# Kernel tuning notes

Measured on AMD Instinct MI355X. Metric: run time of the kernel, lower is better.

The kernel has to match this reference:

```python
import jax, jax.numpy as jnp
import numpy as np

N_NODES = 10000
N_EDGES = 640000
HIDDEN = 128
N_LAYERS = 3
DECAY_RATE = 1.0


def setup_inputs() -> dict:
    key = jax.random.key(0)
    ks = jax.random.split(key, 16)
    D, L = HIDDEN, N_LAYERS
    s = 1.0 / np.sqrt(D)
    inp = {
        "x": jax.random.normal(ks[0], (N_NODES, D), dtype=jnp.float32),
        "edge_index": jax.random.randint(ks[1], (2, N_EDGES), 0, N_NODES, dtype=jnp.int32),
        "confidences": jax.random.uniform(ks[2], (N_NODES,), dtype=jnp.float32),
        # per-layer message MLP params, stacked over layers: [L, D, D] / [L, D]
        "msg_W1": jax.random.normal(ks[3], (L, D, D), dtype=jnp.float32) * s,
        "msg_b1": jnp.zeros((L, D), dtype=jnp.float32),
        "msg_W2": jax.random.normal(ks[4], (L, D, D), dtype=jnp.float32) * s,
        "msg_b2": jnp.zeros((L, D), dtype=jnp.float32),
        # per-layer self MLP params
        "self_W1": jax.random.normal(ks[5], (L, D, D), dtype=jnp.float32) * s,
        "self_b1": jnp.zeros((L, D), dtype=jnp.float32),
        "self_W2": jax.random.normal(ks[6], (L, D, D), dtype=jnp.float32) * s,
        "self_b2": jnp.zeros((L, D), dtype=jnp.float32),
        # layer-importance score net: Linear(D,D) -> ReLU -> Linear(D,1)
        "score_W1": jax.random.normal(ks[7], (D, D), dtype=jnp.float32) * s,
        "score_b1": jnp.zeros((D,), dtype=jnp.float32),
        "score_W2": jax.random.normal(ks[8], (D, 1), dtype=jnp.float32) * s,
        "score_b2": jnp.zeros((1,), dtype=jnp.float32),
    }
    return inp


def _mlp2(h, W1, b1, W2, b2):
    return jax.nn.relu(h @ W1 + b1) @ W2 + b2


def reference(x, edge_index, confidences,
              msg_W1, msg_b1, msg_W2, msg_b2,
              self_W1, self_b1, self_W2, self_b2,
              score_W1, score_b1, score_W2, score_b2):
    src, dst = edge_index[0], edge_index[1]
    # confidence-weighted edge weights: exp(-decay * |c_src - c_dst|)
    edge_weights = jnp.exp(-DECAY_RATE * jnp.abs(confidences[src] - confidences[dst]))  # [E]

    h = x
    layer_outputs = []
    for i in range(N_LAYERS):
        messages = _mlp2(h[src], msg_W1[i], msg_b1[i], msg_W2[i], msg_b2[i])  # [E, D]
        messages = messages * edge_weights[:, None]
        aggr = jax.ops.segment_sum(messages, dst, num_segments=N_NODES)  # [N, D]
        self_loop = _mlp2(h, self_W1[i], self_b1[i], self_W2[i], self_b2[i])
        h = jax.nn.relu(aggr + self_loop)  # dropout is identity in eval mode
        layer_outputs.append(h)

    stacked = jnp.stack(layer_outputs, axis=0)  # [L, N, D]
    scores = _mlp2(stacked, score_W1, score_b1, score_W2, score_b2)[..., 0]  # [L, N]
    layer_weights = jax.nn.softmax(scores, axis=0)  # softmax over layers
    output = jnp.sum(layer_weights[:, :, None] * stacked, axis=0)  # [N, D]
    return output, stacked, layer_weights
```

## Files before the change

kernel.cpp:

```cpp
#include <hip/hip_runtime.h>
#include <hip/hip_fp16.h>

#define NN 10000
#define NE 640000
#define D 128
#define NF (NN * D)
#define WS 136
#define CAP 128
#define GMB 157
#define GE ((NE + 255) / 256)
#define NAGG (NN / 4)
#define NDZ ((NN + 255) / 256)

typedef __bf16 bf16x8 __attribute__((ext_vector_type(8)));
typedef float f32x4 __attribute__((ext_vector_type(4)));


__global__ __launch_bounds__(256) void prep_kernel(
    const float* __restrict__ mW1, const float* __restrict__ mW2,
    const float* __restrict__ sW1, const float* __restrict__ sW2,
    const float* __restrict__ scW1, __bf16* __restrict__ wt, int* __restrict__ deg) {
    int b = blockIdx.x, t = threadIdx.x;
    if (b < 13) {
        int m = b;
        const float* W = (m < 3)   ? mW1 + (size_t)m * D * D
                       : (m < 6)   ? mW2 + (size_t)(m - 3) * D * D
                       : (m < 9)   ? sW1 + (size_t)(m - 6) * D * D
                       : (m < 12)  ? sW2 + (size_t)(m - 9) * D * D
                                   : scW1;
        __bf16* o = wt + (size_t)m * D * WS;
        for (int i = t; i < D * D; i += 256) {
            int k = i >> 7, n = i & 127;
            o[n * WS + k] = (__bf16)W[i];
        }
    } else {
        int i = (b - 13) * 256 + t;
        if (i < NN) deg[i] = 0;
    }
}


__device__ __forceinline__ void mlp_nostage_body(
    const __bf16* __restrict__ Abf, const float* __restrict__ Af32,
    const __bf16* __restrict__ Wt1, const float* __restrict__ b1,
    const __bf16* __restrict__ Wt2, const float* __restrict__ b2,
    __bf16* __restrict__ Mbf, float* __restrict__ Cself, int write_bf,
    __bf16 (*Tl)[16 * WS], int bx, int t) {
    int wid = t >> 6, lane = t & 63;
    int m16 = lane & 15, q = lane >> 4;
    int row0 = bx * 64 + wid * 16;
    int arow = min(row0 + m16, NN - 1);

    bf16x8 af[4];
    if (Af32) {
#pragma unroll
        for (int kk = 0; kk < 4; kk++) {
            const float4* pa = (const float4*)&Af32[(size_t)arow * D + kk * 32 + q * 8];
            float4 v0 = pa[0], v1 = pa[1];
            bf16x8 f;
            f[0] = (__bf16)v0.x; f[1] = (__bf16)v0.y; f[2] = (__bf16)v0.z; f[3] = (__bf16)v0.w;
            f[4] = (__bf16)v1.x; f[5] = (__bf16)v1.y; f[6] = (__bf16)v1.z; f[7] = (__bf16)v1.w;
            af[kk] = f;
        }
    } else {
#pragma unroll
        for (int kk = 0; kk < 4; kk++)
            af[kk] = *(const bf16x8*)&Abf[(size_t)arow * D + kk * 32 + q * 8];
    }
    float b1v[8], b2v[8];
#pragma unroll
    for (int ct = 0; ct < 8; ct++) { b1v[ct] = b1[ct * 16 + m16]; b2v[ct] = b2[ct * 16 + m16]; }

    f32x4 acc[8];
#pragma unroll
    for (int ct = 0; ct < 8; ct++) acc[ct] = (f32x4){0.f, 0.f, 0.f, 0.f};
#pragma unroll
    for (int kk = 0; kk < 4; kk++) {
#pragma unroll
        for (int ct = 0; ct < 8; ct++) {
            bf16x8 bb = *(const bf16x8*)&Wt1[(ct * 16 + m16) * WS + kk * 32 + q * 8];
            acc[ct] = __builtin_amdgcn_mfma_f32_16x16x32_bf16(af[kk], bb, acc[ct], 0, 0, 0);
        }
    }
#pragma unroll
    for (int ct = 0; ct < 8; ct++) {
#pragma unroll
        for (int r = 0; r < 4; r++) {
            float v = fmaxf(acc[ct][r] + b1v[ct], 0.f);
            Tl[wid][(q * 4 + r) * WS + ct * 16 + m16] = (__bf16)v;
        }
    }
#pragma unroll
    for (int ct = 0; ct < 8; ct++) acc[ct] = (f32x4){0.f, 0.f, 0.f, 0.f};
#pragma unroll
    for (int kk = 0; kk < 4; kk++) {
        bf16x8 a = *(const bf16x8*)&Tl[wid][m16 * WS + kk * 32 + q * 8];
#pragma unroll
        for (int ct = 0; ct < 8; ct++) {
            bf16x8 bb = *(const bf16x8*)&Wt2[(ct * 16 + m16) * WS + kk * 32 + q * 8];
            acc[ct] = __builtin_amdgcn_mfma_f32_16x16x32_bf16(a, bb, acc[ct], 0, 0, 0);
        }
    }
    if (write_bf) {
#pragma unroll
        for (int ct = 0; ct < 8; ct++) {
#pragma unroll
            for (int r = 0; r < 4; r++) {
                int row = row0 + q * 4 + r;
                if (row < NN) Mbf[(size_t)row * D + ct * 16 + m16] = (__bf16)(acc[ct][r] + b2v[ct]);
            }
        }
    } else {
#pragma unroll
        for (int ct = 0; ct < 8; ct++) {
#pragma unroll
            for (int r = 0; r < 4; r++) {
                int row = row0 + q * 4 + r;
                if (row < NN) Cself[(size_t)row * D + ct * 16 + m16] = acc[ct][r] + b2v[ct];
            }
        }
    }
}


__global__ __launch_bounds__(256) void scatter_mlp0_kernel(
    const int* __restrict__ ei, const float* __restrict__ conf,
    int* __restrict__ deg, unsigned* __restrict__ meta,
    const float* __restrict__ x,
    const __bf16* __restrict__ wt, const float* __restrict__ b1m, const float* __restrict__ b2m,
    const float* __restrict__ b1s, const float* __restrict__ b2s,
    __bf16* __restrict__ Mbf, float* __restrict__ Cself) {
    __shared__ __align__(16) __bf16 Tl[4][16 * WS];
    const size_t MAT = (size_t)D * WS;
    int b = blockIdx.x, t = threadIdx.x;
    if (b < GE) {
        int e = b * 256 + t;
        if (e < NE) {
            int s = ei[e];
            int d = ei[NE + e];
            float w = expf(-fabsf(conf[s] - conf[d]));
            __half h = __float2half(w);
            unsigned short us = *reinterpret_cast<unsigned short*>(&h);
            unsigned v = ((unsigned)s << 16) | us;
            int r = atomicAdd(&deg[d], 1);
            if (r < CAP) meta[(size_t)d * CAP + r] = v;
        }
        return;
    }
    int mb = b - GE;
    if (mb < GMB)
        mlp_nostage_body(nullptr, x, wt + 0 * MAT, b1m, wt + 3 * MAT, b2m,
                         Mbf, nullptr, 1, Tl, mb, t);
    else
        mlp_nostage_body(nullptr, x, wt + 6 * MAT, b1s, wt + 9 * MAT, b2s,
                         nullptr, Cself, 0, Tl, mb - GMB, t);
}


__device__ __forceinline__ void agg_gather(
    const uint4* __restrict__ Mbf4, const int* __restrict__ deg,
    const unsigned* __restrict__ meta, int wid, int lane, float a[8]) {
    int q = lane >> 4, l4 = lane & 15, l5 = lane & 31;
    int dg = min(deg[wid], CAP);
    size_t beg = (size_t)wid * CAP;
#pragma unroll
    for (int i = 0; i < 8; i++) a[i] = 0.f;
    unsigned mcur = meta[beg + l5];
    for (int rel = 0; rel < dg; rel += 32) {
        unsigned mnext = meta[beg + rel + 32 + l5];
        int srcid[8];
        float wgt[8];
#pragma unroll
        for (int u = 0; u < 8; u++) {
            int sl = 4 * u + q;
            unsigned v = __shfl((int)mcur, sl);
            bool valid = (rel + sl) < dg;
            srcid[u] = valid ? (int)(v >> 16) : 0;
            unsigned short us = (unsigned short)(v & 0xFFFFu);
            __half h = *reinterpret_cast<__half*>(&us);
            wgt[u] = valid ? __half2float(h) : 0.f;
        }
        uint4 g[8];
#pragma unroll
        for (int u = 0; u < 8; u++) g[u] = Mbf4[(size_t)srcid[u] * 16 + l4];
#pragma unroll
        for (int u = 0; u < 8; u++) {
            float w = wgt[u];
            a[0] = fmaf(w, __uint_as_float(g[u].x << 16), a[0]);
            a[1] = fmaf(w, __uint_as_float(g[u].x & 0xFFFF0000u), a[1]);
            a[2] = fmaf(w, __uint_as_float(g[u].y << 16), a[2]);
            a[3] = fmaf(w, __uint_as_float(g[u].y & 0xFFFF0000u), a[3]);
            a[4] = fmaf(w, __uint_as_float(g[u].z << 16), a[4]);
            a[5] = fmaf(w, __uint_as_float(g[u].z & 0xFFFF0000u), a[5]);
            a[6] = fmaf(w, __uint_as_float(g[u].w << 16), a[6]);
            a[7] = fmaf(w, __uint_as_float(g[u].w & 0xFFFF0000u), a[7]);
        }
        mcur = mnext;
    }
#pragma unroll
    for (int i = 0; i < 8; i++) {
        a[i] += __shfl_xor(a[i], 16);
        a[i] += __shfl_xor(a[i], 32);
    }
}


__global__ __launch_bounds__(256) void aggregate_kernel(
    const uint4* __restrict__ Mbf4, const float4* __restrict__ Mself4,
    const int* __restrict__ deg, const unsigned* __restrict__ meta,
    float4* __restrict__ out4, bf16x8* __restrict__ stbf8) {
    int wid = (blockIdx.x * 256 + threadIdx.x) >> 6;
    int lane = threadIdx.x & 63;
    int q = lane >> 4, l4 = lane & 15;
    float a[8];
    agg_gather(Mbf4, deg, meta, wid, lane, a);
    if (q == 0) {
        float4 sv0 = Mself4[(size_t)wid * 32 + 2 * l4];
        float4 sv1 = Mself4[(size_t)wid * 32 + 2 * l4 + 1];
        float4 r0, r1;
        r0.x = fmaxf(a[0] + sv0.x, 0.f);
        r0.y = fmaxf(a[1] + sv0.y, 0.f);
        r0.z = fmaxf(a[2] + sv0.z, 0.f);
        r0.w = fmaxf(a[3] + sv0.w, 0.f);
        r1.x = fmaxf(a[4] + sv1.x, 0.f);
        r1.y = fmaxf(a[5] + sv1.y, 0.f);
        r1.z = fmaxf(a[6] + sv1.z, 0.f);
        r1.w = fmaxf(a[7] + sv1.w, 0.f);
        out4[(size_t)wid * 32 + 2 * l4] = r0;
        out4[(size_t)wid * 32 + 2 * l4 + 1] = r1;
        bf16x8 hb;
        hb[0] = (__bf16)r0.x; hb[1] = (__bf16)r0.y;
        hb[2] = (__bf16)r0.z; hb[3] = (__bf16)r0.w;
        hb[4] = (__bf16)r1.x; hb[5] = (__bf16)r1.y;
        hb[6] = (__bf16)r1.z; hb[7] = (__bf16)r1.w;
        stbf8[(size_t)wid * 16 + l4] = hb;
    }
}


__global__ __launch_bounds__(256) void mlp_pair_mfma(
    const __bf16* __restrict__ Abf,
    const __bf16* __restrict__ Wt1a, const float* __restrict__ b1a,
    const __bf16* __restrict__ Wt2a, const float* __restrict__ b2a, __bf16* __restrict__ Mbf,
    const __bf16* __restrict__ Wt1b, const float* __restrict__ b1b,
    const __bf16* __restrict__ Wt2b, const float* __restrict__ b2b, float* __restrict__ Cself) {
    __shared__ __align__(16) __bf16 Tl[4][16 * WS];
    int pb = blockIdx.y;
    mlp_nostage_body(Abf, nullptr,
                     pb ? Wt1b : Wt1a, pb ? b1b : b1a,
                     pb ? Wt2b : Wt2a, pb ? b2b : b2a,
                     Mbf, Cself, pb == 0, Tl, blockIdx.x, threadIdx.x);
}


__global__ __launch_bounds__(256) void score_finalize_mfma(
    const __bf16* __restrict__ stbf, const float* __restrict__ st,
    const __bf16* __restrict__ Wt1, const float* __restrict__ b1,
    const float* __restrict__ w2, const float* __restrict__ b2,
    float* __restrict__ out, float* __restrict__ lw_out) {
    __shared__ float sc_l[3][64];
    __shared__ float lw_l[3][64];
    int t = threadIdx.x;
    int wid = t >> 6, lane = t & 63;
    int m16 = lane & 15, q = lane >> 4;
    int row0 = blockIdx.x * 64;

    int arow = min(row0 + wid * 16 + m16, NN - 1);
    float bb = b2[0];

    for (int l = 0; l < 3; l++) {
        const __bf16* A = stbf + (size_t)l * NF;
        f32x4 acc[8];
#pragma unroll
        for (int ct = 0; ct < 8; ct++) acc[ct] = (f32x4){0.f, 0.f, 0.f, 0.f};
#pragma unroll
        for (int kk = 0; kk < 4; kk++) {
            bf16x8 a = *(const bf16x8*)&A[(size_t)arow * D + kk * 32 + q * 8];
#pragma unroll
            for (int ct = 0; ct < 8; ct++) {
                bf16x8 b = *(const bf16x8*)&Wt1[(ct * 16 + m16) * WS + kk * 32 + q * 8];
                acc[ct] = __builtin_amdgcn_mfma_f32_16x16x32_bf16(a, b, acc[ct], 0, 0, 0);
            }
        }
        float p[4] = {0.f, 0.f, 0.f, 0.f};
#pragma unroll
        for (int ct = 0; ct < 8; ct++) {
            float bv = b1[ct * 16 + m16];
            float wv = w2[ct * 16 + m16];
#pragma unroll
            for (int r = 0; r < 4; r++) p[r] += fmaxf(acc[ct][r] + bv, 0.f) * wv;
        }
#pragma unroll
        for (int r = 0; r < 4; r++) {
#pragma unroll
            for (int off = 1; off < 16; off <<= 1) p[r] += __shfl_xor(p[r], off);
            if (m16 == 0) sc_l[l][wid * 16 + q * 4 + r] = p[r] + bb;
        }
    }
    __syncthreads();

    if (t < 64) {
        int row = row0 + t;
        float s0 = sc_l[0][t], s1 = sc_l[1][t], s2 = sc_l[2][t];
        float m = fmaxf(s0, fmaxf(s1, s2));
        float e0 = expf(s0 - m), e1 = expf(s1 - m), e2 = expf(s2 - m);
        float inv = 1.f / (e0 + e1 + e2);
        lw_l[0][t] = e0 * inv;
        lw_l[1][t] = e1 * inv;
        lw_l[2][t] = e2 * inv;
        if (row < NN) {
            lw_out[row] = e0 * inv;
            lw_out[NN + row] = e1 * inv;
            lw_out[2 * NN + row] = e2 * inv;
        }
    }
    __syncthreads();

    for (int i = t; i < 64 * 32; i += 256) {
        int r = i >> 5, c4 = i & 31;
        int row = row0 + r;
        if (row >= NN) break;
        float4 v0 = ((const float4*)(st + (size_t)row * D))[c4];
        float4 v1 = ((const float4*)(st + (size_t)NF + (size_t)row * D))[c4];
        float4 v2 = ((const float4*)(st + 2 * (size_t)NF + (size_t)row * D))[c4];
        float w0 = lw_l[0][r], w1 = lw_l[1][r], w2v = lw_l[2][r];
        float4 o;
        o.x = w0 * v0.x + w1 * v1.x + w2v * v2.x;
        o.y = w0 * v0.y + w1 * v1.y + w2v * v2.y;
        o.z = w0 * v0.z + w1 * v1.z + w2v * v2.z;
        o.w = w0 * v0.w + w1 * v1.w + w2v * v2.w;
        ((float4*)(out + (size_t)row * D))[c4] = o;
    }
}

extern "C" void kernel_launch(void* const* d_in, const int* in_sizes, int n_in,
                              void* d_out, int out_size, void* d_ws, size_t ws_size,
                              hipStream_t stream) {
    const float* x = (const float*)d_in[0];
    const int* ei = (const int*)d_in[1];
    const float* conf = (const float*)d_in[2];
    const float* msg_W1 = (const float*)d_in[3];
    const float* msg_b1 = (const float*)d_in[4];
    const float* msg_W2 = (const float*)d_in[5];
    const float* msg_b2 = (const float*)d_in[6];
    const float* self_W1 = (const float*)d_in[7];
    const float* self_b1 = (const float*)d_in[8];
    const float* self_W2 = (const float*)d_in[9];
    const float* self_b2 = (const float*)d_in[10];
    const float* score_W1 = (const float*)d_in[11];
    const float* score_b1 = (const float*)d_in[12];
    const float* score_W2 = (const float*)d_in[13];
    const float* score_b2 = (const float*)d_in[14];

    float* out = (float*)d_out;
    float* out_stacked = out + NF;
    float* out_lw = out + 4 * (size_t)NF;

    float* w = (float*)d_ws;
    float* Mself = w;
    unsigned* meta = (unsigned*)(Mself + (size_t)NF);
    __bf16* stbf = (__bf16*)(meta + (size_t)NN * CAP + 64);
    __bf16* Mbf = stbf + 3 * (size_t)NF;
    __bf16* wt = Mbf + (size_t)NF;
    int* deg = (int*)(wt + 13 * (size_t)D * WS);

    const size_t MAT = (size_t)D * WS;

    prep_kernel<<<13 + NDZ, 256, 0, stream>>>(
        msg_W1, msg_W2, self_W1, self_W2, score_W1, wt, deg);
    scatter_mlp0_kernel<<<GE + 2 * GMB, 256, 0, stream>>>(
        ei, conf, deg, meta, x, wt, msg_b1, msg_b2, self_b1, self_b2, Mbf, Mself);
    aggregate_kernel<<<NAGG, 256, 0, stream>>>(
        (const uint4*)Mbf, (const float4*)Mself, deg, meta,
        (float4*)(out_stacked + 0 * (size_t)NF), (bf16x8*)(stbf + 0 * (size_t)NF));
    mlp_pair_mfma<<<dim3(GMB, 2), 256, 0, stream>>>(
        stbf + 0 * (size_t)NF,
        wt + 1 * MAT, msg_b1 + D, wt + 4 * MAT, msg_b2 + D, Mbf,
        wt + 7 * MAT, self_b1 + D, wt + 10 * MAT, self_b2 + D, Mself);
    aggregate_kernel<<<NAGG, 256, 0, stream>>>(
        (const uint4*)Mbf, (const float4*)Mself, deg, meta,
        (float4*)(out_stacked + 1 * (size_t)NF), (bf16x8*)(stbf + 1 * (size_t)NF));
    mlp_pair_mfma<<<dim3(GMB, 2), 256, 0, stream>>>(
        stbf + 1 * (size_t)NF,
        wt + 2 * MAT, msg_b1 + 2 * D, wt + 5 * MAT, msg_b2 + 2 * D, Mbf,
        wt + 8 * MAT, self_b1 + 2 * D, wt + 11 * MAT, self_b2 + 2 * D, Mself);
    aggregate_kernel<<<NAGG, 256, 0, stream>>>(
        (const uint4*)Mbf, (const float4*)Mself, deg, meta,
        (float4*)(out_stacked + 2 * (size_t)NF), (bf16x8*)(stbf + 2 * (size_t)NF));
    score_finalize_mfma<<<GMB, 256, 0, stream>>>(
        stbf, out_stacked, wt + 12 * MAT, score_b1, score_W2, score_b2, out, out_lw);
}
```

Measured before the change: 271.2 us.

## Fuse message and self MLPs per block and store full-precision edge metadata

Each block now runs both the message MLP and the self MLP on the same input rows, so the A fragment is loaded and converted once instead of twice, and the launch grid is halved. In the first kernel the MLP blocks now come before the edge-scatter blocks. The edge metadata changes from a packed 16-bit source plus fp16 weight to a float2 holding the source id and an fp32 weight. This removes the half-precision conversion but doubles the metadata footprint read during every aggregation.

```diff
diff --git a/kernel.cpp b/kernel.cpp
--- a/kernel.cpp
+++ b/kernel.cpp
@@ -1,5 +1,4 @@
 #include <hip/hip_runtime.h>
-#include <hip/hip_fp16.h>
 
 #define NN 10000
 #define NE 640000
@@ -40,11 +39,74 @@
 }
 
 
-__device__ __forceinline__ void mlp_nostage_body(
-    const __bf16* __restrict__ Abf, const float* __restrict__ Af32,
+__device__ __forceinline__ void mlp_half(
+    const bf16x8 af[4],
     const __bf16* __restrict__ Wt1, const float* __restrict__ b1,
     const __bf16* __restrict__ Wt2, const float* __restrict__ b2,
     __bf16* __restrict__ Mbf, float* __restrict__ Cself, int write_bf,
+    __bf16* Tlw, int row0, int m16, int q) {
+    float b1v[8], b2v[8];
+#pragma unroll
+    for (int ct = 0; ct < 8; ct++) { b1v[ct] = b1[ct * 16 + m16]; b2v[ct] = b2[ct * 16 + m16]; }
+
+    f32x4 acc[8];
+#pragma unroll
+    for (int ct = 0; ct < 8; ct++) acc[ct] = (f32x4){0.f, 0.f, 0.f, 0.f};
+#pragma unroll
+    for (int kk = 0; kk < 4; kk++) {
+#pragma unroll
+        for (int ct = 0; ct < 8; ct++) {
+            bf16x8 bb = *(const bf16x8*)&Wt1[(ct * 16 + m16) * WS + kk * 32 + q * 8];
+            acc[ct] = __builtin_amdgcn_mfma_f32_16x16x32_bf16(af[kk], bb, acc[ct], 0, 0, 0);
+        }
+    }
+#pragma unroll
+    for (int ct = 0; ct < 8; ct++) {
+#pragma unroll
+        for (int r = 0; r < 4; r++) {
+            float v = fmaxf(acc[ct][r] + b1v[ct], 0.f);
+            Tlw[(q * 4 + r) * WS + ct * 16 + m16] = (__bf16)v;
+        }
+    }
+#pragma unroll
+    for (int ct = 0; ct < 8; ct++) acc[ct] = (f32x4){0.f, 0.f, 0.f, 0.f};
+#pragma unroll
+    for (int kk = 0; kk < 4; kk++) {
+        bf16x8 a = *(const bf16x8*)&Tlw[m16 * WS + kk * 32 + q * 8];
+#pragma unroll
+        for (int ct = 0; ct < 8; ct++) {
+            bf16x8 bb = *(const bf16x8*)&Wt2[(ct * 16 + m16) * WS + kk * 32 + q * 8];
+            acc[ct] = __builtin_amdgcn_mfma_f32_16x16x32_bf16(a, bb, acc[ct], 0, 0, 0);
+        }
+    }
+    if (write_bf) {
+#pragma unroll
+        for (int ct = 0; ct < 8; ct++) {
+#pragma unroll
+            for (int r = 0; r < 4; r++) {
+                int row = row0 + q * 4 + r;
+                if (row < NN) Mbf[(size_t)row * D + ct * 16 + m16] = (__bf16)(acc[ct][r] + b2v[ct]);
+            }
+        }
+    } else {
+#pragma unroll
+        for (int ct = 0; ct < 8; ct++) {
+#pragma unroll
+            for (int r = 0; r < 4; r++) {
+                int row = row0 + q * 4 + r;
+                if (row < NN) Cself[(size_t)row * D + ct * 16 + m16] = acc[ct][r] + b2v[ct];
+            }
+        }
+    }
+}
+
+
+__device__ __forceinline__ void mlp_dual_body(
+    const __bf16* __restrict__ Abf, const float* __restrict__ Af32,
+    const __bf16* __restrict__ Wt1m, const float* __restrict__ b1m,
+    const __bf16* __restrict__ Wt2m, const float* __restrict__ b2m, __bf16* __restrict__ Mbf,
+    const __bf16* __restrict__ Wt1s, const float* __restrict__ b1s,
+    const __bf16* __restrict__ Wt2s, const float* __restrict__ b2s, float* __restrict__ Cself,
     __bf16 (*Tl)[16 * WS], int bx, int t) {
     int wid = t >> 6, lane = t & 63;
     int m16 = lane & 15, q = lane >> 4;
@@ -67,65 +129,14 @@
         for (int kk = 0; kk < 4; kk++)
             af[kk] = *(const bf16x8*)&Abf[(size_t)arow * D + kk * 32 + q * 8];
     }
-    float b1v[8], b2v[8];
-#pragma unroll
-    for (int ct = 0; ct < 8; ct++) { b1v[ct] = b1[ct * 16 + m16]; b2v[ct] = b2[ct * 16 + m16]; }
-
-    f32x4 acc[8];
-#pragma unroll
-    for (int ct = 0; ct < 8; ct++) acc[ct] = (f32x4){0.f, 0.f, 0.f, 0.f};
-#pragma unroll
-    for (int kk = 0; kk < 4; kk++) {
-#pragma unroll
-        for (int ct = 0; ct < 8; ct++) {
-            bf16x8 bb = *(const bf16x8*)&Wt1[(ct * 16 + m16) * WS + kk * 32 + q * 8];
-            acc[ct] = __builtin_amdgcn_mfma_f32_16x16x32_bf16(af[kk], bb, acc[ct], 0, 0, 0);
-        }
-    }
-#pragma unroll
-    for (int ct = 0; ct < 8; ct++) {
-#pragma unroll
-        for (int r = 0; r < 4; r++) {
-            float v = fmaxf(acc[ct][r] + b1v[ct], 0.f);
-            Tl[wid][(q * 4 + r) * WS + ct * 16 + m16] = (__bf16)v;
-        }
-    }
-#pragma unroll
-    for (int ct = 0; ct < 8; ct++) acc[ct] = (f32x4){0.f, 0.f, 0.f, 0.f};
-#pragma unroll
-    for (int kk = 0; kk < 4; kk++) {
-        bf16x8 a = *(const bf16x8*)&Tl[wid][m16 * WS + kk * 32 + q * 8];
-#pragma unroll
-        for (int ct = 0; ct < 8; ct++) {
-            bf16x8 bb = *(const bf16x8*)&Wt2[(ct * 16 + m16) * WS + kk * 32 + q * 8];
-            acc[ct] = __builtin_amdgcn_mfma_f32_16x16x32_bf16(a, bb, acc[ct], 0, 0, 0);
-        }
-    }
-    if (write_bf) {
-#pragma unroll
-        for (int ct = 0; ct < 8; ct++) {
-#pragma unroll
-            for (int r = 0; r < 4; r++) {
-                int row = row0 + q * 4 + r;
-                if (row < NN) Mbf[(size_t)row * D + ct * 16 + m16] = (__bf16)(acc[ct][r] + b2v[ct]);
-            }
-        }
-    } else {
-#pragma unroll
-        for (int ct = 0; ct < 8; ct++) {
-#pragma unroll
-            for (int r = 0; r < 4; r++) {
-                int row = row0 + q * 4 + r;
-                if (row < NN) Cself[(size_t)row * D + ct * 16 + m16] = acc[ct][r] + b2v[ct];
-            }
-        }
-    }
+    mlp_half(af, Wt1m, b1m, Wt2m, b2m, Mbf, nullptr, 1, Tl[wid], row0, m16, q);
+    mlp_half(af, Wt1s, b1s, Wt2s, b2s, nullptr, Cself, 0, Tl[wid], row0, m16, q);
 }
 
 
 __global__ __launch_bounds__(256) void scatter_mlp0_kernel(
     const int* __restrict__ ei, const float* __restrict__ conf,
-    int* __restrict__ deg, unsigned* __restrict__ meta,
+    int* __restrict__ deg, float2* __restrict__ meta,
     const float* __restrict__ x,
     const __bf16* __restrict__ wt, const float* __restrict__ b1m, const float* __restrict__ b2m,
     const float* __restrict__ b1s, const float* __restrict__ b2s,
@@ -133,52 +144,44 @@
     __shared__ __align__(16) __bf16 Tl[4][16 * WS];
     const size_t MAT = (size_t)D * WS;
     int b = blockIdx.x, t = threadIdx.x;
-    if (b < GE) {
-        int e = b * 256 + t;
-        if (e < NE) {
-            int s = ei[e];
-            int d = ei[NE + e];
-            float w = expf(-fabsf(conf[s] - conf[d]));
-            __half h = __float2half(w);
-            unsigned short us = *reinterpret_cast<unsigned short*>(&h);
-            unsigned v = ((unsigned)s << 16) | us;
-            int r = atomicAdd(&deg[d], 1);
-            if (r < CAP) meta[(size_t)d * CAP + r] = v;
-        }
+    if (b < GMB) {
+        mlp_dual_body(nullptr, x,
+                      wt + 0 * MAT, b1m, wt + 3 * MAT, b2m, Mbf,
+                      wt + 6 * MAT, b1s, wt + 9 * MAT, b2s, Cself, Tl, b, t);
         return;
     }
-    int mb = b - GE;
-    if (mb < GMB)
-        mlp_nostage_body(nullptr, x, wt + 0 * MAT, b1m, wt + 3 * MAT, b2m,
-                         Mbf, nullptr, 1, Tl, mb, t);
-    else
-        mlp_nostage_body(nullptr, x, wt + 6 * MAT, b1s, wt + 9 * MAT, b2s,
-                         nullptr, Cself, 0, Tl, mb - GMB, t);
+    int e = (b - GMB) * 256 + t;
+    if (e < NE) {
+        int s = ei[e];
+        int d = ei[NE + e];
+        float w = expf(-fabsf(conf[s] - conf[d]));
+        int r = atomicAdd(&deg[d], 1);
+        if (r < CAP) meta[(size_t)d * CAP + r] = make_float2(__int_as_float(s), w);
+    }
 }
 
 
 __device__ __forceinline__ void agg_gather(
     const uint4* __restrict__ Mbf4, const int* __restrict__ deg,
-    const unsigned* __restrict__ meta, int wid, int lane, float a[8]) {
+    const float2* __restrict__ meta, int wid, int lane, float a[8]) {
     int q = lane >> 4, l4 = lane & 15, l5 = lane & 31;
     int dg = min(deg[wid], CAP);
     size_t beg = (size_t)wid * CAP;
 #pragma unroll
     for (int i = 0; i < 8; i++) a[i] = 0.f;
-    unsigned mcur = meta[beg + l5];
+    float2 mcur = meta[beg + l5];
     for (int rel = 0; rel < dg; rel += 32) {
-        unsigned mnext = meta[beg + rel + 32 + l5];
+        float2 mnext = meta[beg + rel + 32 + l5];
         int srcid[8];
         float wgt[8];
 #pragma unroll
         for (int u = 0; u < 8; u++) {
             int sl = 4 * u + q;
-            unsigned v = __shfl((int)mcur, sl);
+            int sid = __float_as_int(__shfl(mcur.x, sl));
+            float w = __shfl(mcur.y, sl);
             bool valid = (rel + sl) < dg;
-            srcid[u] = valid ? (int)(v >> 16) : 0;
-            unsigned short us = (unsigned short)(v & 0xFFFFu);
-            __half h = *reinterpret_cast<__half*>(&us);
-            wgt[u] = valid ? __half2float(h) : 0.f;
+            srcid[u] = valid ? sid : 0;
+            wgt[u] = valid ? w : 0.f;
         }
         uint4 g[8];
 #pragma unroll
@@ -207,7 +210,7 @@
 
 __global__ __launch_bounds__(256) void aggregate_kernel(
     const uint4* __restrict__ Mbf4, const float4* __restrict__ Mself4,
-    const int* __restrict__ deg, const unsigned* __restrict__ meta,
+    const int* __restrict__ deg, const float2* __restrict__ meta,
     float4* __restrict__ out4, bf16x8* __restrict__ stbf8) {
     int wid = (blockIdx.x * 256 + threadIdx.x) >> 6;
     int lane = threadIdx.x & 63;
@@ -238,18 +241,15 @@
 }
 
 
-__global__ __launch_bounds__(256) void mlp_pair_mfma(
+__global__ __launch_bounds__(256) void mlp_dual_mfma(
     const __bf16* __restrict__ Abf,
-    const __bf16* __restrict__ Wt1a, const float* __restrict__ b1a,
-    const __bf16* __restrict__ Wt2a, const float* __restrict__ b2a, __bf16* __restrict__ Mbf,
-    const __bf16* __restrict__ Wt1b, const float* __restrict__ b1b,
-    const __bf16* __restrict__ Wt2b, const float* __restrict__ b2b, float* __restrict__ Cself) {
+    const __bf16* __restrict__ Wt1m, const float* __restrict__ b1m,
+    const __bf16* __restrict__ Wt2m, const float* __restrict__ b2m, __bf16* __restrict__ Mbf,
+    const __bf16* __restrict__ Wt1s, const float* __restrict__ b1s,
+    const __bf16* __restrict__ Wt2s, const float* __restrict__ b2s, float* __restrict__ Cself) {
     __shared__ __align__(16) __bf16 Tl[4][16 * WS];
-    int pb = blockIdx.y;
-    mlp_nostage_body(Abf, nullptr,
-                     pb ? Wt1b : Wt1a, pb ? b1b : b1a,
-                     pb ? Wt2b : Wt2a, pb ? b2b : b2a,
-                     Mbf, Cself, pb == 0, Tl, blockIdx.x, threadIdx.x);
+    mlp_dual_body(Abf, nullptr, Wt1m, b1m, Wt2m, b2m, Mbf,
+                  Wt1s, b1s, Wt2s, b2s, Cself, Tl, blockIdx.x, threadIdx.x);
 }
 
 
@@ -358,7 +358,7 @@
 
     float* w = (float*)d_ws;
     float* Mself = w;
-    unsigned* meta = (unsigned*)(Mself + (size_t)NF);
+    float2* meta = (float2*)(Mself + (size_t)NF);
     __bf16* stbf = (__bf16*)(meta + (size_t)NN * CAP + 64);
     __bf16* Mbf = stbf + 3 * (size_t)NF;
     __bf16* wt = Mbf + (size_t)NF;
@@ -368,19 +368,19 @@
 
     prep_kernel<<<13 + NDZ, 256, 0, stream>>>(
         msg_W1, msg_W2, self_W1, self_W2, score_W1, wt, deg);
-    scatter_mlp0_kernel<<<GE + 2 * GMB, 256, 0, stream>>>(
+    scatter_mlp0_kernel<<<GMB + GE, 256, 0, stream>>>(
         ei, conf, deg, meta, x, wt, msg_b1, msg_b2, self_b1, self_b2, Mbf, Mself);
     aggregate_kernel<<<NAGG, 256, 0, stream>>>(
         (const uint4*)Mbf, (const float4*)Mself, deg, meta,
         (float4*)(out_stacked + 0 * (size_t)NF), (bf16x8*)(stbf + 0 * (size_t)NF));
-    mlp_pair_mfma<<<dim3(GMB, 2), 256, 0, stream>>>(
+    mlp_dual_mfma<<<GMB, 256, 0, stream>>>(
         stbf + 0 * (size_t)NF,
         wt + 1 * MAT, msg_b1 + D, wt + 4 * MAT, msg_b2 + D, Mbf,
         wt + 7 * MAT, self_b1 + D, wt + 10 * MAT, self_b2 + D, Mself);
     aggregate_kernel<<<NAGG, 256, 0, stream>>>(
         (const uint4*)Mbf, (const float4*)Mself, deg, meta,
         (float4*)(out_stacked + 1 * (size_t)NF), (bf16x8*)(stbf + 1 * (size_t)NF));
-    mlp_pair_mfma<<<dim3(GMB, 2), 256, 0, stream>>>(
+    mlp_dual_mfma<<<GMB, 256, 0, stream>>>(
         stbf + 1 * (size_t)NF,
         wt + 2 * MAT, msg_b1 + 2 * D, wt + 5 * MAT, msg_b2 + 2 * D, Mbf,
         wt + 8 * MAT, self_b1 + 2 * D, wt + 11 * MAT, self_b2 + 2 * D, Mself);
```

New measurement: 267.9 us. Within noise of the previous version (-1.2%).
